# Kernel optimization log

Measured on AMD Instinct MI355X. Metric: run time of the kernel, lower is better.

The kernel has to match this reference:

```python
import jax, jax.numpy as jnp
import numpy as np

B, S, D, E, F = 2, 1024, 1024, 14, 2048

def setup_inputs() -> dict:
    key = jax.random.key(0)
    k0, k1, k2, k3 = jax.random.split(key, 4)
    h = jax.random.normal(k0, (B, S, D), jnp.float32)
    gate_w = jax.random.normal(k1, (E, D), jnp.float32) * 0.02
    # kaiming-uniform-ish scale for expert weights
    w1 = jax.random.normal(k2, (E, D, F), jnp.float32) * (1.0 / np.sqrt(D).astype(np.float32))
    b1 = jnp.zeros((E, F), jnp.float32)
    w2 = jax.random.normal(k3, (E, F, D), jnp.float32) * (1.0 / np.sqrt(F).astype(np.float32))
    b2 = jnp.zeros((E, D), jnp.float32)
    return {"h": h, "gate_w": gate_w, "w1": w1, "b1": b1, "w2": w2, "b2": b2}

def reference(h, gate_w, w1, b1, w2, b2):
    # Eval-mode forward (no expert dropout, router_step=None, return_aux=False path)
    Bb, Ss, Dd = h.shape
    x = h.reshape(Bb * Ss, Dd)                       # (N, D)
    logits = x @ gate_w.T                            # (N, E)
    probs = jax.nn.softmax(logits, axis=-1)
    top2_p, top2_i = jax.lax.top_k(probs, 2)         # (N, 2)
    w = top2_p / jnp.maximum(top2_p.sum(-1, keepdims=True), 1e-10)
    # dense all-experts FFN
    hh = jnp.einsum('nd,edf->nef', x, w1) + b1       # (N, E, F)
    hh = jax.nn.gelu(hh, approximate=False)          # torch F.gelu default = exact erf
    all_out = jnp.einsum('nef,efd->ned', hh, w2) + b2  # (N, E, D)
    n = jnp.arange(x.shape[0])
    out0 = all_out[n, top2_i[:, 0]]                  # (N, D)
    out1 = all_out[n, top2_i[:, 1]]
    moe_out = w[:, 0:1] * out0 + w[:, 1:2] * out1
    result = jnp.clip(x + moe_out, -100.0, 100.0).reshape(Bb, Ss, Dd)
    return result
```

## Files before the change

### kernel.cpp

```cpp
#include <hip/hip_runtime.h>
#include <cstdint>
#include <cstddef>

#define NTOK 2048
#define DDIM 1024
#define FDIM 2048
#define NEXP 14
#define MAXT 2048
#define BM   160

typedef __attribute__((ext_vector_type(8))) short short8;
typedef __attribute__((ext_vector_type(4))) float floatx4;

__device__ __forceinline__ unsigned pack2bf(float lo, float hi) {
    unsigned a = __float_as_uint(lo), b = __float_as_uint(hi);
    return ((a + 0x8000u) >> 16) | ((b + 0x8000u) & 0xffff0000u);
}
__device__ __forceinline__ unsigned short f2bf1(float f) {
    return (unsigned short)((__float_as_uint(f) + 0x8000u) >> 16);
}

__device__ __forceinline__ void glds16(const void* g, void* lds) {
    __builtin_amdgcn_global_load_lds((const __attribute__((address_space(1))) unsigned*)g,
                                     (__attribute__((address_space(3))) unsigned*)lds, 16, 0, 0);
}

__device__ __forceinline__ int bswz(int n) { return ((n >> 2) ^ n ^ (n >> 4)) & 7; }

#define SBAR() __builtin_amdgcn_sched_barrier(0)

__global__ __launch_bounds__(256) void cvtx_kernel(const float* __restrict__ x,
                                                   unsigned short* __restrict__ xb,
                                                   int* __restrict__ cnt) {
    if (blockIdx.x == 0 && threadIdx.x < NEXP) cnt[threadIdx.x] = 0;
    const size_t i = ((size_t)blockIdx.x * 256 + threadIdx.x) * 8;
    float4 a = *(const float4*)(x + i);
    float4 b = *(const float4*)(x + i + 4);
    uint4 u;
    u.x = pack2bf(a.x, a.y); u.y = pack2bf(a.z, a.w);
    u.z = pack2bf(b.x, b.y); u.w = pack2bf(b.z, b.w);
    *(uint4*)(xb + i) = u;
}

__global__ __launch_bounds__(256) void gate_kernel(
    const float* __restrict__ x, const float* __restrict__ gw,
    int* __restrict__ cnt, int* __restrict__ lists, float* __restrict__ wt)
{
    const int wave = threadIdx.x >> 6, lane = threadIdx.x & 63;
    const int n = blockIdx.x * 4 + wave;
    float part[NEXP];
#pragma unroll
    for (int e = 0; e < NEXP; ++e) part[e] = 0.f;
    const float4* xr = (const float4*)(x + (size_t)n * DDIM);
#pragma unroll
    for (int kk = 0; kk < 4; ++kk) {
        const float4 xv = xr[kk * 64 + lane];
#pragma unroll
        for (int e = 0; e < NEXP; ++e) {
            const float4 g = ((const float4*)(gw + e * DDIM))[kk * 64 + lane];
            part[e] = fmaf(xv.x, g.x, fmaf(xv.y, g.y, fmaf(xv.z, g.z, fmaf(xv.w, g.w, part[e]))));
        }
    }
#pragma unroll
    for (int e = 0; e < NEXP; ++e) {
        float v = part[e];
        for (int off = 32; off; off >>= 1) v += __shfl_xor(v, off);
        part[e] = v;
    }
    int i0 = 0; float l0 = part[0];
#pragma unroll
    for (int e = 1; e < NEXP; ++e) if (part[e] > l0) { l0 = part[e]; i0 = e; }
    int i1 = -1; float l1 = -3.0e38f;
#pragma unroll
    for (int e = 0; e < NEXP; ++e) if (e != i0 && part[e] > l1) { l1 = part[e]; i1 = e; }
    if (lane == 0) {
        const float r  = __expf(l1 - l0);
        wt[2 * n]     = 1.f / (1.f + r);
        wt[2 * n + 1] = r / (1.f + r);
        int p0 = atomicAdd(&cnt[i0], 1); lists[i0 * MAXT + p0] = 2 * n;
        int p1 = atomicAdd(&cnt[i1], 1); lists[i1 * MAXT + p1] = 2 * n + 1;
    }
}

#define MAXJOBS 40
__global__ void jobs_kernel(const int* __restrict__ cnt, int* __restrict__ job_e,
                            int* __restrict__ job_mt, int* __restrict__ njobs) {
    if (threadIdx.x == 0) {
        int J = 0;
        for (int e = 0; e < NEXP; ++e) {
            const int m = (cnt[e] + BM - 1) / BM;
            for (int i = 0; i < m; ++i) { job_e[J] = e; job_mt[J] = i; ++J; }
        }
        njobs[0] = J;
    }
}

#define LOADB(dst, kbase, STRIDE) {                                           \
    _Pragma("unroll") for (int jj = 0; jj < 8; ++jj)                          \
        dst[jj] = *(const floatx4*)(bG + (size_t)((kbase) + kg * 8 + jj) * (STRIDE)); }

#define WRITEB(src, buf) {                                                    \
    _Pragma("unroll") for (int nn = 0; nn < 4; ++nn) {                        \
        const int n_ = n4 + nn, slot_ = kg ^ bswz(n_);                        \
        uint4 u_;                                                             \
        u_.x = pack2bf(src[0][nn], src[1][nn]); u_.y = pack2bf(src[2][nn], src[3][nn]); \
        u_.z = pack2bf(src[4][nn], src[5][nn]); u_.w = pack2bf(src[6][nn], src[7][nn]); \
        *(uint4*)&Bs[buf][n_ * 64 + slot_ * 8] = u_; } }

#define STAGEA(buf, koff) {                                                   \
    _Pragma("unroll") for (int q = 0; q < 5; ++q)                             \
        glds16(aGp[q] + (koff), &As[buf][(wave * 40 + q * 8) * 64]); }

#define COMPUTE(buf) {                                                        \
    _Pragma("unroll") for (int ks = 0; ks < 2; ++ks) {                        \
        const int c_ = ks * 4 + lq;                                           \
        short8 af[5], bf[4];                                                  \
        _Pragma("unroll") for (int ii = 0; ii < 5; ++ii) {                    \
            const int r_ = wm + ii * 16 + lrow;                               \
            af[ii] = *(const short8*)&As[buf][r_ * 64 + ((c_ ^ (r_ & 7)) * 8)]; } \
        _Pragma("unroll") for (int jn = 0; jn < 4; ++jn) {                    \
            const int n_ = wn + jn * 16 + lrow;                               \
            bf[jn] = *(const short8*)&Bs[buf][n_ * 64 + ((c_ ^ bswz(n_)) * 8)]; } \
        __builtin_amdgcn_s_setprio(1);                                        \
        _Pragma("unroll") for (int ii = 0; ii < 5; ++ii)                      \
            _Pragma("unroll") for (int jn = 0; jn < 4; ++jn)                  \
                acc[ii][jn] = __builtin_amdgcn_mfma_f32_16x16x32_bf16(af[ii], bf[jn], acc[ii][jn], 0, 0, 0); \
        __builtin_amdgcn_s_setprio(0); } }

#define STEADY(i, curbuf, brv_c, brv_n, STRIDE) {                             \
    STAGEA((curbuf) ^ 1, ((i) + 1) * 64);                                     \
    WRITEB(brv_c, (curbuf) ^ 1);                                              \
    SBAR();                                                                   \
    LOADB(brv_n, ((i) + 2) * 64, STRIDE);                                     \
    SBAR();                                                                   \
    COMPUTE(curbuf);                                                          \
    asm volatile("s_waitcnt vmcnt(8) lgkmcnt(0)" ::: "memory");               \
    __builtin_amdgcn_s_barrier(); }

__global__ __launch_bounds__(256, 2) void gemm1_kernel(
    const unsigned short* __restrict__ xb, const float* __restrict__ w1,
    const float* __restrict__ b1, const int* __restrict__ cnt,
    const int* __restrict__ lists, const int* __restrict__ job_e,
    const int* __restrict__ job_mt, const int* __restrict__ njobs,
    unsigned short* __restrict__ hh)
{
    const int j = blockIdx.y;
    if (j >= njobs[0]) return;
    const int e = job_e[j], mt = job_mt[j], nt = blockIdx.x;
    const int count = cnt[e];
    const int* list = lists + e * MAXT + mt * BM;
    const int mloc = min(BM, count - mt * BM);

    __shared__ __align__(16) unsigned short As[2][BM * 64];
    __shared__ __align__(16) unsigned short Bs[2][128 * 64];

    const int t = threadIdx.x, lane = t & 63, wave = t >> 6;
    const int lrow = lane & 15, lq = lane >> 4;
    const int wm = (wave & 1) * 80, wn = (wave >> 1) * 64;

    const int achk = (lane & 7) ^ (lane >> 3);
    const unsigned short* aGp[5];
#pragma unroll
    for (int q = 0; q < 5; ++q) {
        const int r = wave * 40 + q * 8 + (lane >> 3);
        aGp[q] = xb + (size_t)(list[min(r, mloc - 1)] >> 1) * DDIM + achk * 8;
    }

    const int n4 = (t & 31) * 4, kg = t >> 5;
    const float* bG = w1 + (size_t)e * DDIM * FDIM + nt * 128 + n4;

    floatx4 acc[5][4];
#pragma unroll
    for (int ii = 0; ii < 5; ++ii)
#pragma unroll
        for (int jn = 0; jn < 4; ++jn) acc[ii][jn] = (floatx4)0.f;

    floatx4 brvA[8], brvB[8];

    STAGEA(0, 0);
    SBAR();
    LOADB(brvB, 0, FDIM);
    WRITEB(brvB, 0);
    SBAR();
    LOADB(brvA, 64, FDIM);
    asm volatile("s_waitcnt vmcnt(8) lgkmcnt(0)" ::: "memory");
    __builtin_amdgcn_s_barrier();

#pragma unroll 1
    for (int it = 0; it < 7; ++it) {
        const int i = it * 2;
        STEADY(i, 0, brvA, brvB, FDIM);
        STEADY(i + 1, 1, brvB, brvA, FDIM);
    }
    STAGEA(1, 15 * 64);
    WRITEB(brvA, 1);
    SBAR();
    COMPUTE(0);
    asm volatile("s_waitcnt vmcnt(0) lgkmcnt(0)" ::: "memory");
    __builtin_amdgcn_s_barrier();
    COMPUTE(1);

#pragma unroll
    for (int jn = 0; jn < 4; ++jn) {
        const int n = nt * 128 + wn + jn * 16 + lrow;
        const float bias = b1[e * FDIM + n];
#pragma unroll
        for (int ii = 0; ii < 5; ++ii) {
#pragma unroll
            for (int r = 0; r < 4; ++r) {
                const int m = wm + ii * 16 + lq * 4 + r;
                if (m < mloc) {
                    const int pp = list[m];
                    float v = acc[ii][jn][r] + bias;
                    v = 0.5f * v * (1.0f + erff(v * 0.70710678118654752f));
                    hh[(size_t)pp * FDIM + n] = f2bf1(v);
                }
            }
        }
    }
}

__global__ __launch_bounds__(256, 2) void gemm2_kernel(
    const unsigned short* __restrict__ hh, const float* __restrict__ w2,
    const float* __restrict__ b2, const int* __restrict__ cnt,
    const int* __restrict__ lists, const int* __restrict__ job_e,
    const int* __restrict__ job_mt, const int* __restrict__ njobs,
    const float* __restrict__ wt, float* __restrict__ out0, float* __restrict__ out1)
{
    const int j = blockIdx.y;
    if (j >= njobs[0]) return;
    const int e = job_e[j], mt = job_mt[j], nt = blockIdx.x;
    const int count = cnt[e];
    const int* list = lists + e * MAXT + mt * BM;
    const int mloc = min(BM, count - mt * BM);

    __shared__ __align__(16) unsigned short As[2][BM * 64];
    __shared__ __align__(16) unsigned short Bs[2][128 * 64];

    const int t = threadIdx.x, lane = t & 63, wave = t >> 6;
    const int lrow = lane & 15, lq = lane >> 4;
    const int wm = (wave & 1) * 80, wn = (wave >> 1) * 64;

    const int achk = (lane & 7) ^ (lane >> 3);
    const unsigned short* aGp[5];
#pragma unroll
    for (int q = 0; q < 5; ++q) {
        const int r = wave * 40 + q * 8 + (lane >> 3);
        aGp[q] = hh + (size_t)list[min(r, mloc - 1)] * FDIM + achk * 8;
    }

    const int n4 = (t & 31) * 4, kg = t >> 5;
    const float* bG = w2 + (size_t)e * FDIM * DDIM + nt * 128 + n4;

    floatx4 acc[5][4];
#pragma unroll
    for (int ii = 0; ii < 5; ++ii)
#pragma unroll
        for (int jn = 0; jn < 4; ++jn) acc[ii][jn] = (floatx4)0.f;

    floatx4 brvA[8], brvB[8];

    STAGEA(0, 0);
    SBAR();
    LOADB(brvB, 0, DDIM);
    WRITEB(brvB, 0);
    SBAR();
    LOADB(brvA, 64, DDIM);
    asm volatile("s_waitcnt vmcnt(8) lgkmcnt(0)" ::: "memory");
    __builtin_amdgcn_s_barrier();

#pragma unroll 1
    for (int it = 0; it < 15; ++it) {
        const int i = it * 2;
        STEADY(i, 0, brvA, brvB, DDIM);
        STEADY(i + 1, 1, brvB, brvA, DDIM);
    }
    STAGEA(1, 31 * 64);
    WRITEB(brvA, 1);
    SBAR();
    COMPUTE(0);
    asm volatile("s_waitcnt vmcnt(0) lgkmcnt(0)" ::: "memory");
    __builtin_amdgcn_s_barrier();
    COMPUTE(1);

#pragma unroll
    for (int jn = 0; jn < 4; ++jn) {
        const int n = nt * 128 + wn + jn * 16 + lrow;
        const float bias = b2[e * DDIM + n];
#pragma unroll
        for (int ii = 0; ii < 5; ++ii) {
#pragma unroll
            for (int r = 0; r < 4; ++r) {
                const int m = wm + ii * 16 + lq * 4 + r;
                if (m < mloc) {
                    const int pp = list[m];
                    const int tok = pp >> 1;
                    const float v = (acc[ii][jn][r] + bias) * wt[pp];
                    float* dst = (pp & 1) ? out1 : out0;
                    dst[(size_t)tok * DDIM + n] = v;
                }
            }
        }
    }
}

__global__ __launch_bounds__(256) void finalize_kernel(
    const float* __restrict__ x, const float* __restrict__ o1,
    float* __restrict__ out)
{
    const size_t i = ((size_t)blockIdx.x * 256 + threadIdx.x) * 4;
    float4 xv = *(const float4*)(x + i);
    float4 a  = *(const float4*)(out + i);
    float4 b  = *(const float4*)(o1 + i);
    float4 r;
    r.x = fminf(fmaxf(xv.x + a.x + b.x, -100.f), 100.f);
    r.y = fminf(fmaxf(xv.y + a.y + b.y, -100.f), 100.f);
    r.z = fminf(fmaxf(xv.z + a.z + b.z, -100.f), 100.f);
    r.w = fminf(fmaxf(xv.w + a.w + b.w, -100.f), 100.f);
    *(float4*)(out + i) = r;
}

extern "C" void kernel_launch(void* const* d_in, const int* in_sizes, int n_in,
                              void* d_out, int out_size, void* d_ws, size_t ws_size,
                              hipStream_t stream) {
    const float* h  = (const float*)d_in[0];
    const float* gw = (const float*)d_in[1];
    const float* w1 = (const float*)d_in[2];
    const float* b1 = (const float*)d_in[3];
    const float* w2 = (const float*)d_in[4];
    const float* b2 = (const float*)d_in[5];
    float* out = (float*)d_out;

    char* ws = (char*)d_ws;
    int*   cnt    = (int*)ws;
    int*   lists  = (int*)(ws + 256);
    float* wt     = (float*)(ws + 114944);
    int*   job_e  = (int*)(ws + 131328);
    int*   job_mt = (int*)(ws + 131840);
    int*   njobs  = (int*)(ws + 132352);
    unsigned short* xb = (unsigned short*)(ws + 262144);
    float* o1     = (float*)(ws + 262144 + 4194304);
    unsigned short* hhb = (unsigned short*)(ws + 262144 + 4194304 + 8388608);

    cvtx_kernel<<<NTOK * DDIM / (256 * 8), 256, 0, stream>>>(h, xb, cnt);
    gate_kernel<<<NTOK / 4, 256, 0, stream>>>(h, gw, cnt, lists, wt);
    jobs_kernel<<<1, 64, 0, stream>>>(cnt, job_e, job_mt, njobs);
    gemm1_kernel<<<dim3(FDIM / 128, MAXJOBS), 256, 0, stream>>>(xb, w1, b1, cnt, lists, job_e, job_mt, njobs, hhb);
    gemm2_kernel<<<dim3(DDIM / 128, MAXJOBS), 256, 0, stream>>>(hhb, w2, b2, cnt, lists, job_e, job_mt, njobs, wt, out, o1);
    finalize_kernel<<<NTOK * DDIM / (256 * 4), 256, 0, stream>>>(h, o1, out);
}
```

Baseline: 419.9 us.

## Split-K gemm2 with atomic accumulation and triple-buffered register B prefetch

The second expert GEMM now splits its K dimension (F) in two across a new grid z-dimension. This doubles the number of blocks for better occupancy and load balance, and partial sums are combined with atomicAdd into pre-zeroed outputs. The outputs are zeroed inside the conversion kernel. Both GEMMs also move from a two-register-buffer B prefetch to three buffers, keeping loads two stages ahead to hide global latency. The cost is extra atomic traffic, extra zeroing writes, more registers, and results that may vary slightly between runs.

```diff
diff --git a/kernel.cpp b/kernel.cpp
--- a/kernel.cpp
+++ b/kernel.cpp
@@ -31,15 +31,21 @@
 
 __global__ __launch_bounds__(256) void cvtx_kernel(const float* __restrict__ x,
                                                    unsigned short* __restrict__ xb,
-                                                   int* __restrict__ cnt) {
+                                                   int* __restrict__ cnt,
+                                                   float* __restrict__ out0z,
+                                                   float* __restrict__ o1z) {
     if (blockIdx.x == 0 && threadIdx.x < NEXP) cnt[threadIdx.x] = 0;
-    const size_t i = ((size_t)blockIdx.x * 256 + threadIdx.x) * 8;
+    const size_t tid = (size_t)blockIdx.x * 256 + threadIdx.x;
+    const size_t i = tid * 8;
     float4 a = *(const float4*)(x + i);
     float4 b = *(const float4*)(x + i + 4);
     uint4 u;
     u.x = pack2bf(a.x, a.y); u.y = pack2bf(a.z, a.w);
     u.z = pack2bf(b.x, b.y); u.w = pack2bf(b.z, b.w);
     *(uint4*)(xb + i) = u;
+    float4 z = {0.f, 0.f, 0.f, 0.f};
+    *(float4*)(out0z + i) = z; *(float4*)(out0z + i + 4) = z;
+    *(float4*)(o1z + i) = z;   *(float4*)(o1z + i + 4) = z;
 }
 
 __global__ __launch_bounds__(256) void gate_kernel(
@@ -127,15 +133,47 @@
                 acc[ii][jn] = __builtin_amdgcn_mfma_f32_16x16x32_bf16(af[ii], bf[jn], acc[ii][jn], 0, 0, 0); \
         __builtin_amdgcn_s_setprio(0); } }
 
-#define STEADY(i, curbuf, brv_c, brv_n, STRIDE) {                             \
-    STAGEA((curbuf) ^ 1, ((i) + 1) * 64);                                     \
-    WRITEB(brv_c, (curbuf) ^ 1);                                              \
-    SBAR();                                                                   \
-    LOADB(brv_n, ((i) + 2) * 64, STRIDE);                                     \
-    SBAR();                                                                   \
-    COMPUTE(curbuf);                                                          \
+#define STEP_FULL(i, Rw, Rl, STRIDE) {                                        \
+    STAGEA(((i) + 1) & 1, ((i) + 1) * 64);                                    \
+    WRITEB(Rw, ((i) + 1) & 1);                                                \
+    SBAR();                                                                   \
+    LOADB(Rl, ((i) + 3) * 64, STRIDE);                                        \
+    SBAR();                                                                   \
+    COMPUTE((i) & 1);                                                         \
     asm volatile("s_waitcnt vmcnt(8) lgkmcnt(0)" ::: "memory");               \
     __builtin_amdgcn_s_barrier(); }
+
+#define STEP_NOLOAD(i, Rw) {                                                  \
+    STAGEA(((i) + 1) & 1, ((i) + 1) * 64);                                    \
+    WRITEB(Rw, ((i) + 1) & 1);                                                \
+    SBAR();                                                                   \
+    COMPUTE((i) & 1);                                                         \
+    asm volatile("s_waitcnt vmcnt(0) lgkmcnt(0)" ::: "memory");               \
+    __builtin_amdgcn_s_barrier(); }
+
+#define GEMM_PROLOGUE(STRIDE) {                                               \
+    LOADB(brv0, 0, STRIDE);                                                   \
+    STAGEA(0, 0);                                                             \
+    WRITEB(brv0, 0);                                                          \
+    SBAR();                                                                   \
+    LOADB(brv1, 64, STRIDE);                                                  \
+    LOADB(brv2, 128, STRIDE);                                                 \
+    SBAR();                                                                   \
+    asm volatile("s_waitcnt vmcnt(16) lgkmcnt(0)" ::: "memory");              \
+    __builtin_amdgcn_s_barrier(); }
+
+#define GEMM_MAINLOOP(STRIDE) {                                               \
+    _Pragma("unroll 1")                                                       \
+    for (int g = 0; g < 4; ++g) {                                             \
+        const int i = g * 3;                                                  \
+        STEP_FULL(i,     brv1, brv0, STRIDE);                                 \
+        STEP_FULL(i + 1, brv2, brv1, STRIDE);                                 \
+        STEP_FULL(i + 2, brv0, brv2, STRIDE);                                 \
+    }                                                                         \
+    STEP_FULL(12, brv1, brv0, STRIDE);                                        \
+    STEP_NOLOAD(13, brv2);                                                    \
+    STEP_NOLOAD(14, brv0);                                                    \
+    COMPUTE(1); }
 
 __global__ __launch_bounds__(256, 2) void gemm1_kernel(
     const unsigned short* __restrict__ xb, const float* __restrict__ w1,
@@ -175,30 +213,10 @@
 #pragma unroll
         for (int jn = 0; jn < 4; ++jn) acc[ii][jn] = (floatx4)0.f;
 
-    floatx4 brvA[8], brvB[8];
-
-    STAGEA(0, 0);
-    SBAR();
-    LOADB(brvB, 0, FDIM);
-    WRITEB(brvB, 0);
-    SBAR();
-    LOADB(brvA, 64, FDIM);
-    asm volatile("s_waitcnt vmcnt(8) lgkmcnt(0)" ::: "memory");
-    __builtin_amdgcn_s_barrier();
-
-#pragma unroll 1
-    for (int it = 0; it < 7; ++it) {
-        const int i = it * 2;
-        STEADY(i, 0, brvA, brvB, FDIM);
-        STEADY(i + 1, 1, brvB, brvA, FDIM);
-    }
-    STAGEA(1, 15 * 64);
-    WRITEB(brvA, 1);
-    SBAR();
-    COMPUTE(0);
-    asm volatile("s_waitcnt vmcnt(0) lgkmcnt(0)" ::: "memory");
-    __builtin_amdgcn_s_barrier();
-    COMPUTE(1);
+    floatx4 brv0[8], brv1[8], brv2[8];
+
+    GEMM_PROLOGUE(FDIM);
+    GEMM_MAINLOOP(FDIM);
 
 #pragma unroll
     for (int jn = 0; jn < 4; ++jn) {
@@ -229,7 +247,7 @@
 {
     const int j = blockIdx.y;
     if (j >= njobs[0]) return;
-    const int e = job_e[j], mt = job_mt[j], nt = blockIdx.x;
+    const int e = job_e[j], mt = job_mt[j], nt = blockIdx.x, sk = blockIdx.z;
     const int count = cnt[e];
     const int* list = lists + e * MAXT + mt * BM;
     const int mloc = min(BM, count - mt * BM);
@@ -246,11 +264,11 @@
 #pragma unroll
     for (int q = 0; q < 5; ++q) {
         const int r = wave * 40 + q * 8 + (lane >> 3);
-        aGp[q] = hh + (size_t)list[min(r, mloc - 1)] * FDIM + achk * 8;
+        aGp[q] = hh + (size_t)list[min(r, mloc - 1)] * FDIM + sk * 1024 + achk * 8;
     }
 
     const int n4 = (t & 31) * 4, kg = t >> 5;
-    const float* bG = w2 + (size_t)e * FDIM * DDIM + nt * 128 + n4;
+    const float* bG = w2 + (size_t)e * FDIM * DDIM + (size_t)sk * 1024 * DDIM + nt * 128 + n4;
 
     floatx4 acc[5][4];
 #pragma unroll
@@ -258,35 +276,15 @@
 #pragma unroll
         for (int jn = 0; jn < 4; ++jn) acc[ii][jn] = (floatx4)0.f;
 
-    floatx4 brvA[8], brvB[8];
-
-    STAGEA(0, 0);
-    SBAR();
-    LOADB(brvB, 0, DDIM);
-    WRITEB(brvB, 0);
-    SBAR();
-    LOADB(brvA, 64, DDIM);
-    asm volatile("s_waitcnt vmcnt(8) lgkmcnt(0)" ::: "memory");
-    __builtin_amdgcn_s_barrier();
-
-#pragma unroll 1
-    for (int it = 0; it < 15; ++it) {
-        const int i = it * 2;
-        STEADY(i, 0, brvA, brvB, DDIM);
-        STEADY(i + 1, 1, brvB, brvA, DDIM);
-    }
-    STAGEA(1, 31 * 64);
-    WRITEB(brvA, 1);
-    SBAR();
-    COMPUTE(0);
-    asm volatile("s_waitcnt vmcnt(0) lgkmcnt(0)" ::: "memory");
-    __builtin_amdgcn_s_barrier();
-    COMPUTE(1);
+    floatx4 brv0[8], brv1[8], brv2[8];
+
+    GEMM_PROLOGUE(DDIM);
+    GEMM_MAINLOOP(DDIM);
 
 #pragma unroll
     for (int jn = 0; jn < 4; ++jn) {
         const int n = nt * 128 + wn + jn * 16 + lrow;
-        const float bias = b2[e * DDIM + n];
+        const float bias = (sk == 0) ? b2[e * DDIM + n] : 0.f;
 #pragma unroll
         for (int ii = 0; ii < 5; ++ii) {
 #pragma unroll
@@ -297,7 +295,7 @@
                     const int tok = pp >> 1;
                     const float v = (acc[ii][jn][r] + bias) * wt[pp];
                     float* dst = (pp & 1) ? out1 : out0;
-                    dst[(size_t)tok * DDIM + n] = v;
+                    atomicAdd(dst + (size_t)tok * DDIM + n, v);
                 }
             }
         }
@@ -342,10 +340,10 @@
     float* o1     = (float*)(ws + 262144 + 4194304);
     unsigned short* hhb = (unsigned short*)(ws + 262144 + 4194304 + 8388608);
 
-    cvtx_kernel<<<NTOK * DDIM / (256 * 8), 256, 0, stream>>>(h, xb, cnt);
+    cvtx_kernel<<<NTOK * DDIM / (256 * 8), 256, 0, stream>>>(h, xb, cnt, out, o1);
     gate_kernel<<<NTOK / 4, 256, 0, stream>>>(h, gw, cnt, lists, wt);
     jobs_kernel<<<1, 64, 0, stream>>>(cnt, job_e, job_mt, njobs);
     gemm1_kernel<<<dim3(FDIM / 128, MAXJOBS), 256, 0, stream>>>(xb, w1, b1, cnt, lists, job_e, job_mt, njobs, hhb);
-    gemm2_kernel<<<dim3(DDIM / 128, MAXJOBS), 256, 0, stream>>>(hhb, w2, b2, cnt, lists, job_e, job_mt, njobs, wt, out, o1);
+    gemm2_kernel<<<dim3(DDIM / 128, MAXJOBS, 2), 256, 0, stream>>>(hhb, w2, b2, cnt, lists, job_e, job_mt, njobs, wt, out, o1);
     finalize_kernel<<<NTOK * DDIM / (256 * 4), 256, 0, stream>>>(h, o1, out);
 }
```

New measurement: 447.2 us. +6.5%, slower.
